# Optimization experiments

Hardware: AMD Instinct MI355X
Metric: run time of the kernel (lower is better)

Reference implementation:

```python
import jax, jax.numpy as jnp
import numpy as np

D = 1024      # input_dim
H = 16        # head_num
HD = 64       # head_dim
HID = 4096    # mlp hidden
CUR = 512     # cur_seq
PREV = 512    # prev_seq (memory)
FULL = CUR + PREV
BS = 16
SCALE = 1.0 / (HD ** 0.5)


def setup_inputs() -> dict:
    key = jax.random.key(0)
    ks = jax.random.split(key, 20)
    def nrm(k, shape, s=0.02):
        return (jax.random.normal(k, shape) * s).astype(jnp.float32)
    inp = {
        "inputs": nrm(ks[0], (CUR, BS, D), 1.0),
        "pos_embedding": nrm(ks[1], (FULL, 1, D), 1.0),
        "u": nrm(ks[2], (H, HD)),
        "v": nrm(ks[3], (H, HD)),
        "memory": nrm(ks[4], (PREV, BS, D), 1.0),
        # causal mask: position i (query) may attend to j <= i + PREV; True = masked
        "mask": jnp.triu(jnp.ones((CUR, FULL), dtype=bool), k=PREV + 1)[:, :, None],
        # attention params (stored as (in, out); torch Linear applies x @ W.T + b)
        "Wkv": nrm(ks[5], (D, 2 * H * HD)), "bkv": jnp.zeros((2 * H * HD,), jnp.float32),
        "Wq": nrm(ks[6], (D, H * HD)), "bq": jnp.zeros((H * HD,), jnp.float32),
        "Wo": nrm(ks[7], (H * HD, D)), "bo": jnp.zeros((D,), jnp.float32),
        "Wp": nrm(ks[8], (D, H * HD)), "bp": jnp.zeros((H * HD,), jnp.float32),
        # layernorms
        "ln1_g": jnp.ones((D,), jnp.float32), "ln1_b": jnp.zeros((D,), jnp.float32),
        "ln2_g": jnp.ones((D,), jnp.float32), "ln2_b": jnp.zeros((D,), jnp.float32),
        # mlp (mlp_num=2): Linear(D,HID)+relu, Linear(HID,D)+relu
        "W1": nrm(ks[9], (D, HID)), "b1": jnp.zeros((HID,), jnp.float32),
        "W2": nrm(ks[10], (HID, D)), "b2": jnp.zeros((D,), jnp.float32),
        # GRU gates: stacked [Wr,Wz,Wg] and [Ur,Uz,Ug], no bias; bg init 2.0
        "g1_W": nrm(ks[11], (3, D, D)), "g1_U": nrm(ks[12], (3, D, D)),
        "g1_bg": jnp.full((D,), 2.0, jnp.float32),
        "g2_W": nrm(ks[13], (3, D, D)), "g2_U": nrm(ks[14], (3, D, D)),
        "g2_bg": jnp.full((D,), 2.0, jnp.float32),
    }
    return inp


def _layernorm(x, g, b, eps=1e-5):
    mu = jnp.mean(x, axis=-1, keepdims=True)
    var = jnp.mean(jnp.square(x - mu), axis=-1, keepdims=True)
    return (x - mu) * jax.lax.rsqrt(var + eps) * g + b


def _rel_shift(x):
    # x: (bs, head, cur, full) -> pad/reshape/slice trick of Transformer-XL
    b, h, c, f = x.shape
    xp = jnp.pad(x, ((0, 0), (0, 0), (0, 0), (1, 0)))      # (b,h,c,f+1)
    xp = xp.reshape(b, h, f + 1, c)
    return xp[:, :, 1:, :].reshape(b, h, c, f)


def _gru_gate(x, y, W, U, bg):
    # W, U: (3, D, D) for [r, z, g] gates; torch Linear => y @ W[i].T
    r = jax.nn.sigmoid(y @ W[0].T + x @ U[0].T)
    z = jax.nn.sigmoid(y @ W[1].T + x @ U[1].T - bg)
    h = jnp.tanh(y @ W[2].T + (r * x) @ U[2].T)
    return (1.0 - z) * x + z * h


def _attention_xl(x_cur, pos_emb, x_full, u, v, mask,
                  Wkv, bkv, Wq, bq, Wo, bo, Wp, bp):
    cur, bs, _ = x_cur.shape
    full = x_full.shape[0]
    kv = x_full @ Wkv + bkv                                  # (full, bs, 2*H*HD)
    key, value = jnp.split(kv, 2, axis=-1)
    query = x_cur @ Wq + bq                                  # (cur, bs, H*HD)
    r = (pos_emb @ Wp + bp).reshape(full, H, HD)             # (full, H, HD)

    key = key.reshape(full, bs, H, HD)
    value = value.reshape(full, bs, H, HD)
    query = query.reshape(cur, bs, H, HD)

    content = jnp.einsum('ibhd,jbhd->bhij', query + u, key)  # (bs,H,cur,full)
    position = jnp.einsum('ibhd,jhd->bhij', query + v, r)    # (bs,H,cur,full)
    position = _rel_shift(position)

    attn = (content + position) * SCALE
    # mask: (cur, full, 1) bool, True = masked
    m = mask[:, :, 0][None, None]                            # (1,1,cur,full)
    attn = jnp.where(m, -jnp.inf, attn)
    p = jax.nn.softmax(attn, axis=-1)

    out = jnp.einsum('bhij,jbhd->ibhd', p, value).reshape(cur, bs, H * HD)
    return out @ Wo + bo                                     # (cur, bs, D)


def reference(inputs, pos_embedding, u, v, memory, mask,
              Wkv, bkv, Wq, bq, Wo, bo, Wp, bp,
              ln1_g, ln1_b, ln2_g, ln2_b,
              W1, b1, W2, b2,
              g1_W, g1_U, g1_bg, g2_W, g2_U, g2_bg):
    prev = memory.shape[0]
    full_input = jnp.concatenate([memory, inputs], axis=0)   # (full, bs, D)
    x1 = _layernorm(full_input, ln1_g, ln1_b)
    a1 = _attention_xl(x1[prev:], pos_embedding, x1, u, v, mask,
                       Wkv, bkv, Wq, bq, Wo, bo, Wp, bp)
    a1 = jax.nn.relu(a1)                                     # dropout = identity (eval)
    o1 = _gru_gate(inputs, a1, g1_W, g1_U, g1_bg)
    x2 = _layernorm(o1, ln2_g, ln2_b)
    m2 = jax.nn.relu(jax.nn.relu(x2 @ W1 + b1) @ W2 + b2)    # mlp: act after every linear
    o2 = _gru_gate(o1, m2, g2_W, g2_U, g2_bg)
    return o2
```

## Files before the change

### kernel.cpp

```cpp
#include <hip/hip_runtime.h>
#include <stdint.h>

typedef _Float16 h16;
typedef __attribute__((ext_vector_type(8))) _Float16 f16x8;
typedef __attribute__((ext_vector_type(4))) _Float16 f16x4;
typedef __attribute__((ext_vector_type(4))) float f32x4;

enum { F_OBF = 1, F_BIAS = 2, F_RELU = 4, F_ACC = 8, F_DUAL = 16 };

#define BARRIER_MEM                                  \
  do {                                               \
    asm volatile("" ::: "memory");                   \
    __builtin_amdgcn_s_barrier();                    \
    asm volatile("" ::: "memory");                   \
  } while (0)

static __device__ __forceinline__ void gload16(const void* g, void* l) {
  __builtin_amdgcn_global_load_lds((__attribute__((address_space(1))) void*)g,
                                   (__attribute__((address_space(3))) void*)l,
                                   16, 0, 0);
}

template <int BN, int FLAGS>
__global__ __launch_bounds__(512) void gemm2_k(
    const h16* __restrict__ A, const h16* __restrict__ B,
    void* __restrict__ Cv, const float* __restrict__ bias,
    int K, int lda, int ldb, int ldc, int gm,
    void* __restrict__ C2v, const float* __restrict__ bias2) {
  constexpr int NH = BN / 128;
  constexpr int WN = BN / 4;
  __shared__ h16 Al[2][256][64];
  __shared__ h16 Bl[2][BN][64];

  const int tid = threadIdx.x, lane = tid & 63, wid = tid >> 6;
  const int wr = wid >> 2, wn = wid & 3;
  const int ar = lane & 15, q4 = lane >> 4;

  const int nwg = gridDim.x, cpx = nwg >> 3;
  const int bid = (blockIdx.x & 7) * cpx + (blockIdx.x >> 3);
  const int mx = bid % gm, ny = bid / gm;

  const h16* Ab = A + (long)mx * 256 * lda;
  const h16* Bb = B + (long)ny * BN * ldb;

  auto stageA = [&](int buf, int half, int k0) {
#pragma unroll
    for (int l = 0; l < 2; ++l) {
      const int idx = l * 512 + tid;
      const int row = half * 128 + (idx >> 3), sl = idx & 7;
      gload16(Ab + (long)row * lda + k0 + (sl ^ (row & 7)) * 8,
              (char*)&Al[buf][0][0] + (half * 1024 + l * 512 + wid * 64) * 16);
    }
  };
  auto stageB = [&](int buf, int half, int k0) {
#pragma unroll
    for (int l = 0; l < NH; ++l) {
      const int idx = l * 512 + tid;
      const int row = half * (BN / 2) + (idx >> 3), sl = idx & 7;
      gload16(Bb + (long)row * ldb + k0 + (sl ^ (row & 7)) * 8,
              (char*)&Bl[buf][0][0] + (half * (BN * 4) + l * 512 + wid * 64) * 16);
    }
  };

  f32x4 acc[8][2 * NH] = {};
  const int nk = K >> 6;

  stageB(0, 0, 0); stageB(0, 1, 0); stageA(0, 0, 0); stageA(0, 1, 0);
  if (nk > 1) { stageB(1, 0, 64); stageB(1, 1, 64); stageA(1, 0, 64); stageA(1, 1, 64); }
  if (nk > 1) {
    if constexpr (NH == 2) asm volatile("s_waitcnt vmcnt(8)" ::: "memory");
    else                   asm volatile("s_waitcnt vmcnt(6)" ::: "memory");
  } else {
    asm volatile("s_waitcnt vmcnt(0)" ::: "memory");
  }
  BARRIER_MEM;

  for (int kt = 0; kt < nk; ++kt) {
    const int b = kt & 1;
    const int k2 = (kt + 2) << 6;
    const bool pf = (kt + 2) < nk;

    f16x8 a0[4][2], b0[NH][2];
#pragma unroll
    for (int m = 0; m < 4; ++m) {
      const int row = wr * 128 + m * 16 + ar;
#pragma unroll
      for (int ks = 0; ks < 2; ++ks)
        a0[m][ks] = *(const f16x8*)&Al[b][row][((ks * 4 + q4) ^ (row & 7)) * 8];
    }
#pragma unroll
    for (int n = 0; n < NH; ++n) {
      const int row = wn * WN + n * 16 + ar;
#pragma unroll
      for (int ks = 0; ks < 2; ++ks)
        b0[n][ks] = *(const f16x8*)&Bl[b][row][((ks * 4 + q4) ^ (row & 7)) * 8];
    }
    BARRIER_MEM;
    __builtin_amdgcn_s_setprio(1);
#pragma unroll
    for (int m = 0; m < 4; ++m)
#pragma unroll
      for (int n = 0; n < NH; ++n)
#pragma unroll
        for (int ks = 0; ks < 2; ++ks)
          acc[m][n] = __builtin_amdgcn_mfma_f32_16x16x32_f16(a0[m][ks], b0[n][ks], acc[m][n], 0, 0, 0);
    __builtin_amdgcn_s_setprio(0);
    BARRIER_MEM;

    f16x8 b1f[NH][2];
#pragma unroll
    for (int n = 0; n < NH; ++n) {
      const int row = wn * WN + (n + NH) * 16 + ar;
#pragma unroll
      for (int ks = 0; ks < 2; ++ks)
        b1f[n][ks] = *(const f16x8*)&Bl[b][row][((ks * 4 + q4) ^ (row & 7)) * 8];
    }
    BARRIER_MEM;
    __builtin_amdgcn_s_setprio(1);
#pragma unroll
    for (int m = 0; m < 4; ++m)
#pragma unroll
      for (int n = 0; n < NH; ++n)
#pragma unroll
        for (int ks = 0; ks < 2; ++ks)
          acc[m][n + NH] = __builtin_amdgcn_mfma_f32_16x16x32_f16(a0[m][ks], b1f[n][ks], acc[m][n + NH], 0, 0, 0);
    __builtin_amdgcn_s_setprio(0);
    BARRIER_MEM;

    f16x8 a1f[4][2];
#pragma unroll
    for (int m = 0; m < 4; ++m) {
      const int row = wr * 128 + (m + 4) * 16 + ar;
#pragma unroll
      for (int ks = 0; ks < 2; ++ks)
        a1f[m][ks] = *(const f16x8*)&Al[b][row][((ks * 4 + q4) ^ (row & 7)) * 8];
    }
    if (pf) { stageB(b, 0, k2); stageB(b, 1, k2); }
    BARRIER_MEM;
    __builtin_amdgcn_s_setprio(1);
#pragma unroll
    for (int m = 0; m < 4; ++m)
#pragma unroll
      for (int n = 0; n < NH; ++n)
#pragma unroll
        for (int ks = 0; ks < 2; ++ks)
          acc[m + 4][n] = __builtin_amdgcn_mfma_f32_16x16x32_f16(a1f[m][ks], b0[n][ks], acc[m + 4][n], 0, 0, 0);
    __builtin_amdgcn_s_setprio(0);
    BARRIER_MEM;

    if (pf) { stageA(b, 0, k2); stageA(b, 1, k2); }
    __builtin_amdgcn_s_setprio(1);
#pragma unroll
    for (int m = 0; m < 4; ++m)
#pragma unroll
      for (int n = 0; n < NH; ++n)
#pragma unroll
        for (int ks = 0; ks < 2; ++ks)
          acc[m + 4][n + NH] = __builtin_amdgcn_mfma_f32_16x16x32_f16(a1f[m][ks], b1f[n][ks], acc[m + 4][n + NH], 0, 0, 0);
    __builtin_amdgcn_s_setprio(0);
    if (pf) {
      if constexpr (NH == 2) asm volatile("s_waitcnt vmcnt(8)" ::: "memory");
      else                   asm volatile("s_waitcnt vmcnt(6)" ::: "memory");
    } else if (kt + 1 < nk) {
      asm volatile("s_waitcnt vmcnt(0)" ::: "memory");
    }
    BARRIER_MEM;
  }

#pragma unroll
  for (int m = 0; m < 8; ++m) {
#pragma unroll
    for (int n = 0; n < 2 * NH; ++n) {
      const int col = ny * BN + wn * WN + n * 16 + ar;
      float bv1 = 0.f, bv2 = 0.f;
      if (FLAGS & F_BIAS) bv1 = bias[col];
      if (FLAGS & F_DUAL) bv2 = bias2[col];
#pragma unroll
      for (int r = 0; r < 4; ++r) {
        const int row = mx * 256 + wr * 128 + m * 16 + q4 * 4 + r;
        float val = acc[m][n][r] + bv1;
        if (FLAGS & F_RELU) val = fmaxf(val, 0.f);
        if constexpr ((FLAGS & F_ACC) != 0) {
          float* p = (float*)Cv + (long)row * ldc + col;
          *p = *p + val;
        } else if constexpr ((FLAGS & F_OBF) != 0) {
          ((h16*)Cv)[(long)row * ldc + col] = (h16)val;
          if constexpr ((FLAGS & F_DUAL) != 0)
            ((h16*)C2v)[(long)row * ldc + col] = (h16)(acc[m][n][r] + bv2);
        } else {
          ((float*)Cv)[(long)row * ldc + col] = val;
        }
      }
    }
  }
}

__global__ __launch_bounds__(256) void fattn_k(
    const h16* __restrict__ qu, const h16* __restrict__ qv,
    const h16* __restrict__ kvb, const h16* __restrict__ vT,
    const h16* __restrict__ rb, h16* __restrict__ attn) {
  __shared__ h16 Kl[2][128][64];
  __shared__ h16 Vl[64][128];
  __shared__ h16 Psc[4][16][164];

  const int tid = threadIdx.x, lane = tid & 63, wv = tid >> 6;
  const int z = blockIdx.x, b = z >> 4, h = z & 15;
  const int i0 = blockIdx.y * 64;
  const int ar = lane & 15, q4 = lane >> 4;
  const int myrow = i0 + wv * 16;
  const h16* vTz = vT + (long)z * 64 * 1024;

  const long qoff = ((long)(myrow + ar) * 16 + b) * 1024 + h * 64 + q4 * 8;
  f16x8 quf[2], qvf[2];
  quf[0] = *(const f16x8*)&qu[qoff];
  quf[1] = *(const f16x8*)&qu[qoff + 32];
  qvf[0] = *(const f16x8*)&qv[qoff];
  qvf[1] = *(const f16x8*)&qv[qoff + 32];

  f32x4 o[4] = {};
  float lrow[4] = {0.f, 0.f, 0.f, 0.f};

  const int ntiles = (i0 + 575 + 128) >> 7;

  auto stageK = [&](int buf, int j0) {
#pragma unroll
    for (int it = 0; it < 4; ++it) {
      const int ch = it * 256 + wv * 64 + lane;
      const int kr = ch >> 3, ks = ch & 7;
      gload16(kvb + ((long)(j0 + kr) * 16 + b) * 2048 + h * 64 + (ks ^ (kr & 7)) * 8,
              (char*)&Kl[buf][0][0] + (it * 256 + wv * 64) * 16);
    }
  };
  auto stageV = [&](int j0) {
#pragma unroll
    for (int it = 0; it < 4; ++it) {
      const int ch = it * 256 + wv * 64 + lane;
      const int vd = ch >> 4, vs = ch & 15;
      gload16(vTz + (long)vd * 1024 + j0 + (vs ^ (vd & 7)) * 8,
              (char*)&Vl[0][0] + (it * 256 + wv * 64) * 16);
    }
  };

  stageK(0, 0);
  asm volatile("s_waitcnt vmcnt(0)" ::: "memory");
  __builtin_amdgcn_s_barrier();

  for (int t = 0; t < ntiles; ++t) {
    const int j0 = t * 128;
    const int kb = t & 1;
    const bool pk = (t + 1) < ntiles;

    stageV(j0);
    if (pk) stageK(kb ^ 1, (t + 1) * 128);
    if (pk) asm volatile("s_waitcnt vmcnt(8)" ::: "memory");
    else    asm volatile("s_waitcnt vmcnt(4)" ::: "memory");
    BARRIER_MEM;

    f32x4 acc_c[8] = {};
#pragma unroll
    for (int kd = 0; kd < 2; ++kd)
#pragma unroll
      for (int nf = 0; nf < 8; ++nf) {
        const int j = nf * 16 + ar;
        const int phys = (kd * 4 + q4) ^ (j & 7);
        const f16x8 kf = *(const f16x8*)&Kl[kb][j][phys * 8];
        acc_c[nf] = __builtin_amdgcn_mfma_f32_16x16x32_f16(quf[kd], kf, acc_c[nf], 0, 0, 0);
      }

    const int jbase = j0 - myrow + 496;
    f32x4 acc_p[9] = {};
#pragma unroll
    for (int kd = 0; kd < 2; ++kd)
#pragma unroll
      for (int jf = 0; jf < 9; ++jf) {
        int jjr = jbase + jf * 16 + ar;
        if (jjr > 1023) jjr = 1023;
        const f16x8 rf = *(const f16x8*)&rb[(long)jjr * 1024 + h * 64 + kd * 32 + q4 * 8];
        acc_p[jf] = __builtin_amdgcn_mfma_f32_16x16x32_f16(qvf[kd], rf, acc_p[jf], 0, 0, 0);
      }
#pragma unroll
    for (int jf = 0; jf < 9; ++jf)
#pragma unroll
      for (int r = 0; r < 4; ++r)
        Psc[wv][q4 * 4 + r][jf * 16 + ar] = (h16)acc_p[jf][r];

    float p[8][4];
#pragma unroll
    for (int nf = 0; nf < 8; ++nf)
#pragma unroll
      for (int r = 0; r < 4; ++r) {
        const int iloc = q4 * 4 + r;
        const int jloc = nf * 16 + ar;
        const int band = jloc - iloc + 15;
        const float pv = (float)Psc[wv][iloc][band];
        const float sv = (acc_c[nf][r] + pv) * 0.125f;
        const bool ok = (j0 + jloc) <= (myrow + iloc + 512);
        p[nf][r] = ok ? __expf(sv) : 0.f;
      }
#pragma unroll
    for (int r = 0; r < 4; ++r) {
      float ts = 0.f;
#pragma unroll
      for (int nf = 0; nf < 8; ++nf) ts += p[nf][r];
      ts += __shfl_xor(ts, 1);
      ts += __shfl_xor(ts, 2);
      ts += __shfl_xor(ts, 4);
      ts += __shfl_xor(ts, 8);
      lrow[r] += ts;
    }

#pragma unroll
    for (int nf = 0; nf < 8; ++nf)
#pragma unroll
      for (int r = 0; r < 4; ++r) {
        const int iloc = q4 * 4 + r, jloc = nf * 16 + ar;
        Psc[wv][iloc][((jloc >> 3) ^ (iloc & 7)) * 8 + (jloc & 7)] = (h16)p[nf][r];
      }

    if (pk) asm volatile("s_waitcnt vmcnt(4)" ::: "memory");
    else    asm volatile("s_waitcnt vmcnt(0)" ::: "memory");
    BARRIER_MEM;

#pragma unroll
    for (int ks = 0; ks < 4; ++ks) {
      const f16x8 pa = *(const f16x8*)&Psc[wv][ar][((ks * 4 + q4) ^ (ar & 7)) * 8];
#pragma unroll
      for (int vnf = 0; vnf < 4; ++vnf) {
        const int d = vnf * 16 + ar;
        const f16x8 vb = *(const f16x8*)&Vl[d][((ks * 4 + q4) ^ (d & 7)) * 8];
        o[vnf] = __builtin_amdgcn_mfma_f32_16x16x32_f16(pa, vb, o[vnf], 0, 0, 0);
      }
    }
    BARRIER_MEM;
  }

#pragma unroll
  for (int vnf = 0; vnf < 4; ++vnf)
#pragma unroll
    for (int r = 0; r < 4; ++r) {
      const int i_ = myrow + q4 * 4 + r;
      attn[((long)i_ * 16 + b) * 1024 + h * 64 + vnf * 16 + ar] =
          (h16)(o[vnf][r] / lrow[r]);
    }
}

__global__ __launch_bounds__(256) void wtransM_k(
    const float* __restrict__ Wkv, const float* __restrict__ Wq,
    const float* __restrict__ Wo, const float* __restrict__ Wp,
    const float* __restrict__ W1, const float* __restrict__ W2,
    h16* __restrict__ o0, h16* __restrict__ o1, h16* __restrict__ o2,
    h16* __restrict__ o3, h16* __restrict__ o4, h16* __restrict__ o5) {
  const int seg = blockIdx.y, t = blockIdx.x;
  int gx, gy, N, K;
  const float* in;
  h16* out;
  switch (seg) {
    case 0: gx = 64;  gy = 32;  in = Wkv; out = o0; N = 2048; K = 1024; break;
    case 1: gx = 32;  gy = 32;  in = Wq;  out = o1; N = 1024; K = 1024; break;
    case 2: gx = 32;  gy = 32;  in = Wo;  out = o2; N = 1024; K = 1024; break;
    case 3: gx = 32;  gy = 32;  in = Wp;  out = o3; N = 1024; K = 1024; break;
    case 4: gx = 128; gy = 32;  in = W1;  out = o4; N = 4096; K = 1024; break;
    default: gx = 32; gy = 128; in = W2;  out = o5; N = 1024; K = 4096; break;
  }
  if (t >= gx * gy) return;
  const int n0 = (t % gx) * 32, k0 = (t / gx) * 32;
  __shared__ float tb[32][33];
  const int tx = threadIdx.x & 31, ty = threadIdx.x >> 5;
#pragma unroll
  for (int j = 0; j < 32; j += 8)
    tb[ty + j][tx] = in[(long)(k0 + ty + j) * N + n0 + tx];
  __syncthreads();
#pragma unroll
  for (int j = 0; j < 32; j += 8)
    out[(long)(n0 + ty + j) * K + k0 + tx] = (h16)tb[tx][ty + j];
}

__global__ __launch_bounds__(256) void cast_k(const float* __restrict__ in,
                                              h16* __restrict__ out, long n4) {
  const long i = (long)blockIdx.x * 256 + threadIdx.x;
  if (i >= n4) return;
  const float4 v = ((const float4*)in)[i];
  f16x4 o;
  o[0] = (h16)v.x; o[1] = (h16)v.y; o[2] = (h16)v.z; o[3] = (h16)v.w;
  ((f16x4*)out)[i] = o;
}

__global__ __launch_bounds__(256) void gateprep_k(
    const float* __restrict__ W1g, const float* __restrict__ U1g,
    const float* __restrict__ W2g, const float* __restrict__ U2g,
    h16* __restrict__ o1, h16* __restrict__ o2) {
  const long i = (long)blockIdx.x * 256 + threadIdx.x;
  const long elem = i * 4;
  const int row = (int)(elem >> 11);
  const int col = (int)(elem & 2047);
  const int gate = row >> 10, oc = row & 1023;
  const float* W = (blockIdx.y == 0) ? W1g : W2g;
  const float* U = (blockIdx.y == 0) ? U1g : U2g;
  h16* out = (blockIdx.y == 0) ? o1 : o2;
  const float* src = (col < 1024)
      ? (W + (long)gate * 1048576 + (long)oc * 1024 + col)
      : (U + (long)gate * 1048576 + (long)oc * 1024 + (col - 1024));
  const float4 v = *(const float4*)src;
  f16x4 o;
  o[0] = (h16)v.x; o[1] = (h16)v.y; o[2] = (h16)v.z; o[3] = (h16)v.w;
  *(f16x4*)(out + elem) = o;
}

__global__ __launch_bounds__(256) void xcast_k(const float* __restrict__ in,
                                               h16* __restrict__ yx) {
  const long i = (long)blockIdx.x * 256 + threadIdx.x;
  const long row = i >> 8;
  const int c4 = (int)(i & 255);
  const float4 v = ((const float4*)in)[i];
  f16x4 o;
  o[0] = (h16)v.x; o[1] = (h16)v.y; o[2] = (h16)v.z; o[3] = (h16)v.w;
  *(f16x4*)(yx + row * 2048 + 1024 + c4 * 4) = o;
}

__global__ void addbias_k(const float* __restrict__ bq, const float* __restrict__ u,
                          const float* __restrict__ v, float* __restrict__ qu,
                          float* __restrict__ qv) {
  const int c = blockIdx.x * 256 + threadIdx.x;
  if (c < 1024) { qu[c] = bq[c] + u[c]; qv[c] = bq[c] + v[c]; }
}

__global__ __launch_bounds__(256) void zero_out_k(float* __restrict__ out, long n) {
  const long i = (long)blockIdx.x * 256 + threadIdx.x;
  if (i < n) out[i] = 0.f;
}

__global__ __launch_bounds__(256) void ln_k(const float* __restrict__ src0,
                                            const float* __restrict__ src1, int rows0,
                                            const float* __restrict__ g,
                                            const float* __restrict__ b,
                                            h16* __restrict__ out) {
  const int row = blockIdx.x, tid = threadIdx.x;
  const float* src = (row < rows0) ? (src0 + (long)row * 1024)
                                   : (src1 + (long)(row - rows0) * 1024);
  const float4 x = ((const float4*)src)[tid];
  float s = x.x + x.y + x.z + x.w;
  float sq = x.x * x.x + x.y * x.y + x.z * x.z + x.w * x.w;
#pragma unroll
  for (int o = 32; o > 0; o >>= 1) { s += __shfl_down(s, o); sq += __shfl_down(sq, o); }
  __shared__ float red[8];
  const int lane = tid & 63, w = tid >> 6;
  if (lane == 0) { red[w] = s; red[4 + w] = sq; }
  __syncthreads();
  s = red[0] + red[1] + red[2] + red[3];
  sq = red[4] + red[5] + red[6] + red[7];
  const float mu = s * (1.f / 1024.f);
  const float inv = rsqrtf(sq * (1.f / 1024.f) - mu * mu + 1e-5f);
  const float4 gg = ((const float4*)g)[tid], bb = ((const float4*)b)[tid];
  f16x4 o;
  o[0] = (h16)((x.x - mu) * inv * gg.x + bb.x);
  o[1] = (h16)((x.y - mu) * inv * gg.y + bb.y);
  o[2] = (h16)((x.z - mu) * inv * gg.z + bb.z);
  o[3] = (h16)((x.w - mu) * inv * gg.w + bb.w);
  ((f16x4*)(out + (long)row * 1024))[tid] = o;
}

__global__ __launch_bounds__(256) void vtrans_k(const h16* __restrict__ kv,
                                                h16* __restrict__ vT) {
  const int z = blockIdx.y, b = z >> 4, h = z & 15;
  const int j0 = blockIdx.x * 64;
  __shared__ h16 t[64][72];
  const int jj = threadIdx.x >> 3, c = threadIdx.x & 7;
#pragma unroll
  for (int half = 0; half < 2; ++half) {
    const int j = jj + half * 32;
    const f16x8 v = *(const f16x8*)(kv + ((long)(j0 + j) * 16 + b) * 2048 + 1024 + h * 64 + c * 8);
    *(f16x8*)&t[j][c * 8] = v;
  }
  __syncthreads();
#pragma unroll
  for (int half = 0; half < 2; ++half) {
    const int d = jj + half * 32;
    f16x8 o;
#pragma unroll
    for (int k = 0; k < 8; ++k) o[k] = t[c * 8 + k][d];
    *(f16x8*)(vT + ((long)z * 64 + d) * 1024 + j0 + c * 8) = o;
  }
}

__global__ __launch_bounds__(256) void gru_rx_k(const h16* __restrict__ T,
                                                const float* __restrict__ x,
                                                h16* __restrict__ yx) {
  const long i = (long)blockIdx.x * 256 + threadIdx.x;
  const long row = i >> 8;
  const int c4 = (int)(i & 255);
  const f16x4 t = *(const f16x4*)(T + row * 2048 + c4 * 4);
  const float4 xx = ((const float4*)x)[i];
  f16x4 o;
  o[0] = (h16)(xx.x / (1.f + __expf(-(float)t[0])));
  o[1] = (h16)(xx.y / (1.f + __expf(-(float)t[1])));
  o[2] = (h16)(xx.z / (1.f + __expf(-(float)t[2])));
  o[3] = (h16)(xx.w / (1.f + __expf(-(float)t[3])));
  *(f16x4*)(yx + row * 2048 + 1024 + c4 * 4) = o;
}

__global__ __launch_bounds__(256) void gru_out_k(const h16* __restrict__ T,
                                                 const h16* __restrict__ G,
                                                 const float* __restrict__ x,
                                                 const float* __restrict__ bg,
                                                 float* __restrict__ outf) {
  const long i = (long)blockIdx.x * 256 + threadIdx.x;
  const long row = i >> 8;
  const int c4 = (int)(i & 255);
  const f16x4 tz = *(const f16x4*)(T + row * 2048 + 1024 + c4 * 4);
  const f16x4 th = *(const f16x4*)(G + row * 1024 + c4 * 4);
  const float4 xx = ((const float4*)x)[i];
  const float4 bb = ((const float4*)bg)[c4];
  float4 o;
  {
    const float z0 = 1.f / (1.f + __expf(-((float)tz[0] - bb.x)));
    const float z1 = 1.f / (1.f + __expf(-((float)tz[1] - bb.y)));
    const float z2 = 1.f / (1.f + __expf(-((float)tz[2] - bb.z)));
    const float z3 = 1.f / (1.f + __expf(-((float)tz[3] - bb.w)));
    o.x = (1.f - z0) * xx.x + z0 * tanhf((float)th[0]);
    o.y = (1.f - z1) * xx.y + z1 * tanhf((float)th[1]);
    o.z = (1.f - z2) * xx.z + z2 * tanhf((float)th[2]);
    o.w = (1.f - z3) * xx.w + z3 * tanhf((float)th[3]);
  }
  ((float4*)outf)[i] = o;
}

__global__ __launch_bounds__(256) void gruo_ln_k(
    const h16* __restrict__ T, const h16* __restrict__ G,
    const float* __restrict__ x, const float* __restrict__ bg,
    const float* __restrict__ lng, const float* __restrict__ lnb,
    float* __restrict__ outf, h16* __restrict__ yx2, h16* __restrict__ x2) {
  const int row = blockIdx.x, tid = threadIdx.x;
  const f16x4 tz = *(const f16x4*)(T + (long)row * 2048 + 1024 + tid * 4);
  const f16x4 th = *(const f16x4*)(G + (long)row * 1024 + tid * 4);
  const float4 xx = ((const float4*)(x + (long)row * 1024))[tid];
  const float4 bb = ((const float4*)bg)[tid];
  float4 o;
  {
    const float z0 = 1.f / (1.f + __expf(-((float)tz[0] - bb.x)));
    const float z1 = 1.f / (1.f + __expf(-((float)tz[1] - bb.y)));
    const float z2 = 1.f / (1.f + __expf(-((float)tz[2] - bb.z)));
    const float z3 = 1.f / (1.f + __expf(-((float)tz[3] - bb.w)));
    o.x = (1.f - z0) * xx.x + z0 * tanhf((float)th[0]);
    o.y = (1.f - z1) * xx.y + z1 * tanhf((float)th[1]);
    o.z = (1.f - z2) * xx.z + z2 * tanhf((float)th[2]);
    o.w = (1.f - z3) * xx.w + z3 * tanhf((float)th[3]);
  }
  ((float4*)(outf + (long)row * 1024))[tid] = o;
  {
    f16x4 oh;
    oh[0] = (h16)o.x; oh[1] = (h16)o.y; oh[2] = (h16)o.z; oh[3] = (h16)o.w;
    *(f16x4*)(yx2 + (long)row * 2048 + 1024 + tid * 4) = oh;
  }
  float s = o.x + o.y + o.z + o.w;
  float sq = o.x * o.x + o.y * o.y + o.z * o.z + o.w * o.w;
#pragma unroll
  for (int off = 32; off > 0; off >>= 1) {
    s += __shfl_down(s, off);
    sq += __shfl_down(sq, off);
  }
  __shared__ float red[8];
  const int lane = tid & 63, wvi = tid >> 6;
  if (lane == 0) { red[wvi] = s; red[4 + wvi] = sq; }
  __syncthreads();
  s = red[0] + red[1] + red[2] + red[3];
  sq = red[4] + red[5] + red[6] + red[7];
  const float mu = s * (1.f / 1024.f);
  const float inv = rsqrtf(sq * (1.f / 1024.f) - mu * mu + 1e-5f);
  const float4 gg = ((const float4*)lng)[tid], bn = ((const float4*)lnb)[tid];
  f16x4 ol;
  ol[0] = (h16)((o.x - mu) * inv * gg.x + bn.x);
  ol[1] = (h16)((o.y - mu) * inv * gg.y + bn.y);
  ol[2] = (h16)((o.z - mu) * inv * gg.z + bn.z);
  ol[3] = (h16)((o.w - mu) * inv * gg.w + bn.w);
  *(f16x4*)(x2 + (long)row * 1024 + tid * 4) = ol;
}

extern "C" void kernel_launch(void* const* d_in, const int* in_sizes, int n_in,
                              void* d_out, int out_size, void* d_ws, size_t ws_size,
                              hipStream_t stream) {
  const float* inputs = (const float*)d_in[0];
  const float* pos    = (const float*)d_in[1];
  const float* u      = (const float*)d_in[2];
  const float* v      = (const float*)d_in[3];
  const float* memory = (const float*)d_in[4];
  const float* Wkv = (const float*)d_in[6];  const float* bkv = (const float*)d_in[7];
  const float* Wq  = (const float*)d_in[8];  const float* bq  = (const float*)d_in[9];
  const float* Wo  = (const float*)d_in[10]; const float* bo  = (const float*)d_in[11];
  const float* Wp  = (const float*)d_in[12]; const float* bp  = (const float*)d_in[13];
  const float* ln1_g = (const float*)d_in[14]; const float* ln1_b = (const float*)d_in[15];
  const float* ln2_g = (const float*)d_in[16]; const float* ln2_b = (const float*)d_in[17];
  const float* W1 = (const float*)d_in[18]; const float* b1 = (const float*)d_in[19];
  const float* W2 = (const float*)d_in[20]; const float* b2 = (const float*)d_in[21];
  const float* g1_W = (const float*)d_in[22]; const float* g1_U = (const float*)d_in[23];
  const float* g1_bg = (const float*)d_in[24];
  const float* g2_W = (const float*)d_in[25]; const float* g2_U = (const float*)d_in[26];
  const float* g2_bg = (const float*)d_in[27];
  (void)in_sizes; (void)n_in;

  const size_t MB = 1u << 20;
  const size_t NEEDED = 247 * MB;
  const dim3 blk(256);
  if (ws_size < NEEDED) {
    zero_out_k<<<(out_size + 255) / 256, blk, 0, stream>>>((float*)d_out, out_size);
    return;
  }

  char* w = (char*)d_ws;
  h16* WoT   = (h16*)(w + 0 * MB);
  h16* W1T   = (h16*)(w + 2 * MB);
  h16* W2T   = (h16*)(w + 10 * MB);
  h16* g1B   = (h16*)(w + 18 * MB);
  h16* g2B   = (h16*)(w + 30 * MB);
  h16* WkvT  = (h16*)(w + 42 * MB);
  h16* WqT   = (h16*)(w + 46 * MB);
  h16* WpT   = (h16*)(w + 48 * MB);
  h16* posb  = (h16*)(w + 50 * MB);
  float* bias_qu = (float*)(w + 52 * MB);
  float* bias_qv = (float*)(w + 52 * MB + 8192);
  h16* yx1   = (h16*)(w + 53 * MB);
  h16* x1    = (h16*)(w + 85 * MB);
  char* Rbig =        w + 117 * MB;
  h16* qu    = (h16*)(w + 181 * MB);
  h16* qv    = (h16*)(w + 197 * MB);
  h16* attn  = (h16*)(w + 213 * MB);
  h16* rb    = (h16*)(w + 245 * MB);

  h16*   kvb  = (h16*)Rbig;
  h16*   Trzh = (h16*)Rbig;
  h16*   Tg   = (h16*)(Rbig + 32 * MB);
  h16*   h1   = (h16*)Rbig;
  h16*   vT   = x1;
  h16*   yx2  = x1;
  float* o1f  = (float*)attn;
  h16*   x2   = yx1;

  wtransM_k<<<dim3(4096, 6), blk, 0, stream>>>(Wkv, Wq, Wo, Wp, W1, W2,
                                               WkvT, WqT, WoT, WpT, W1T, W2T);
  gateprep_k<<<dim3(6144, 2), blk, 0, stream>>>(g1_W, g1_U, g2_W, g2_U, g1B, g2B);
  cast_k<<<1024, blk, 0, stream>>>(pos, posb, 262144);
  xcast_k<<<8192, blk, 0, stream>>>(inputs, yx1);
  addbias_k<<<4, blk, 0, stream>>>(bq, u, v, bias_qu, bias_qv);

  ln_k<<<16384, blk, 0, stream>>>(memory, inputs, 8192, ln1_g, ln1_b, x1);

  gemm2_k<256, F_OBF | F_BIAS><<<dim3(512), dim3(512), 0, stream>>>(
      x1, WkvT, kvb, bkv, 1024, 1024, 1024, 2048, 64, nullptr, nullptr);
  gemm2_k<128, F_OBF | F_BIAS | F_DUAL><<<dim3(256), dim3(512), 0, stream>>>(
      x1 + 8192L * 1024, WqT, qu, bias_qu, 1024, 1024, 1024, 1024, 32, qv, bias_qv);
  gemm2_k<128, F_OBF | F_BIAS><<<dim3(32), dim3(512), 0, stream>>>(
      posb, WpT, rb, bp, 1024, 1024, 1024, 1024, 4, nullptr, nullptr);
  vtrans_k<<<dim3(16, 256), blk, 0, stream>>>(kvb, vT);

  fattn_k<<<dim3(256, 8), blk, 0, stream>>>(qu, qv, kvb, vT, rb, attn);

  gemm2_k<128, F_OBF | F_BIAS | F_RELU><<<dim3(256), dim3(512), 0, stream>>>(
      attn, WoT, yx1, bo, 1024, 1024, 1024, 2048, 32, nullptr, nullptr);

  gemm2_k<256, F_OBF><<<dim3(256), dim3(512), 0, stream>>>(
      yx1, g1B, Trzh, nullptr, 2048, 2048, 2048, 2048, 32, nullptr, nullptr);
  gru_rx_k<<<8192, blk, 0, stream>>>(Trzh, inputs, yx1);
  gemm2_k<128, F_OBF><<<dim3(256), dim3(512), 0, stream>>>(
      yx1, g1B + 2048L * 2048, Tg, nullptr, 2048, 2048, 2048, 1024, 32, nullptr, nullptr);
  gruo_ln_k<<<8192, blk, 0, stream>>>(Trzh, Tg, inputs, g1_bg, ln2_g, ln2_b,
                                      o1f, yx2, x2);

  gemm2_k<256, F_OBF | F_BIAS | F_RELU><<<dim3(512), dim3(512), 0, stream>>>(
      x2, W1T, h1, b1, 1024, 1024, 1024, 4096, 32, nullptr, nullptr);
  gemm2_k<128, F_OBF | F_BIAS | F_RELU><<<dim3(256), dim3(512), 0, stream>>>(
      h1, W2T, yx2, b2, 4096, 4096, 4096, 2048, 32, nullptr, nullptr);

  gemm2_k<256, F_OBF><<<dim3(256), dim3(512), 0, stream>>>(
      yx2, g2B, Trzh, nullptr, 2048, 2048, 2048, 2048, 32, nullptr, nullptr);
  gru_rx_k<<<8192, blk, 0, stream>>>(Trzh, o1f, yx2);
  gemm2_k<128, F_OBF><<<dim3(256), dim3(512), 0, stream>>>(
      yx2, g2B + 2048L * 2048, Tg, nullptr, 2048, 2048, 2048, 1024, 32, nullptr, nullptr);
  gru_out_k<<<8192, blk, 0, stream>>>(Trzh, Tg, o1f, g2_bg, (float*)d_out);
}
```

Baseline: 976.8 us.

## Merge prep kernels, store GRU intermediate in fp16, add MFMA priority hints

Combines the pos cast, input cast and bias-add prep kernels into a single launch with a y-segment switch. The first GRU output o1 is now stored as fp16 instead of fp32, which halves the traffic for the second GRU stage reads. The attention kernel raises wave priority around its MFMA loops and pads the score scratch row from 164 to 168 halves. The fp16 intermediate lowers the precision of the residual path in the second GRU.

```diff
diff --git a/kernel.cpp b/kernel.cpp
--- a/kernel.cpp
+++ b/kernel.cpp
@@ -201,7 +201,7 @@
     const h16* __restrict__ rb, h16* __restrict__ attn) {
   __shared__ h16 Kl[2][128][64];
   __shared__ h16 Vl[64][128];
-  __shared__ h16 Psc[4][16][164];
+  __shared__ h16 Psc[4][16][168];
 
   const int tid = threadIdx.x, lane = tid & 63, wv = tid >> 6;
   const int z = blockIdx.x, b = z >> 4, h = z & 15;
@@ -257,6 +257,7 @@
     BARRIER_MEM;
 
     f32x4 acc_c[8] = {};
+    __builtin_amdgcn_s_setprio(1);
 #pragma unroll
     for (int kd = 0; kd < 2; ++kd)
 #pragma unroll
@@ -266,9 +267,11 @@
         const f16x8 kf = *(const f16x8*)&Kl[kb][j][phys * 8];
         acc_c[nf] = __builtin_amdgcn_mfma_f32_16x16x32_f16(quf[kd], kf, acc_c[nf], 0, 0, 0);
       }
+    __builtin_amdgcn_s_setprio(0);
 
     const int jbase = j0 - myrow + 496;
     f32x4 acc_p[9] = {};
+    __builtin_amdgcn_s_setprio(1);
 #pragma unroll
     for (int kd = 0; kd < 2; ++kd)
 #pragma unroll
@@ -278,6 +281,7 @@
         const f16x8 rf = *(const f16x8*)&rb[(long)jjr * 1024 + h * 64 + kd * 32 + q4 * 8];
         acc_p[jf] = __builtin_amdgcn_mfma_f32_16x16x32_f16(qvf[kd], rf, acc_p[jf], 0, 0, 0);
       }
+    __builtin_amdgcn_s_setprio(0);
 #pragma unroll
     for (int jf = 0; jf < 9; ++jf)
 #pragma unroll
@@ -321,6 +325,7 @@
     else    asm volatile("s_waitcnt vmcnt(0)" ::: "memory");
     BARRIER_MEM;
 
+    __builtin_amdgcn_s_setprio(1);
 #pragma unroll
     for (int ks = 0; ks < 4; ++ks) {
       const f16x8 pa = *(const f16x8*)&Psc[wv][ar][((ks * 4 + q4) ^ (ar & 7)) * 8];
@@ -331,6 +336,7 @@
         o[vnf] = __builtin_amdgcn_mfma_f32_16x16x32_f16(pa, vb, o[vnf], 0, 0, 0);
       }
     }
+    __builtin_amdgcn_s_setprio(0);
     BARRIER_MEM;
   }
 
@@ -373,16 +379,6 @@
 #pragma unroll
   for (int j = 0; j < 32; j += 8)
     out[(long)(n0 + ty + j) * K + k0 + tx] = (h16)tb[tx][ty + j];
-}
-
-__global__ __launch_bounds__(256) void cast_k(const float* __restrict__ in,
-                                              h16* __restrict__ out, long n4) {
-  const long i = (long)blockIdx.x * 256 + threadIdx.x;
-  if (i >= n4) return;
-  const float4 v = ((const float4*)in)[i];
-  f16x4 o;
-  o[0] = (h16)v.x; o[1] = (h16)v.y; o[2] = (h16)v.z; o[3] = (h16)v.w;
-  ((f16x4*)out)[i] = o;
 }
 
 __global__ __launch_bounds__(256) void gateprep_k(
@@ -406,22 +402,31 @@
   *(f16x4*)(out + elem) = o;
 }
 
-__global__ __launch_bounds__(256) void xcast_k(const float* __restrict__ in,
-                                               h16* __restrict__ yx) {
-  const long i = (long)blockIdx.x * 256 + threadIdx.x;
-  const long row = i >> 8;
-  const int c4 = (int)(i & 255);
-  const float4 v = ((const float4*)in)[i];
-  f16x4 o;
-  o[0] = (h16)v.x; o[1] = (h16)v.y; o[2] = (h16)v.z; o[3] = (h16)v.w;
-  *(f16x4*)(yx + row * 2048 + 1024 + c4 * 4) = o;
-}
-
-__global__ void addbias_k(const float* __restrict__ bq, const float* __restrict__ u,
-                          const float* __restrict__ v, float* __restrict__ qu,
-                          float* __restrict__ qv) {
-  const int c = blockIdx.x * 256 + threadIdx.x;
-  if (c < 1024) { qu[c] = bq[c] + u[c]; qv[c] = bq[c] + v[c]; }
+__global__ __launch_bounds__(256) void prep2_k(
+    const float* __restrict__ pos, h16* __restrict__ posb,
+    const float* __restrict__ inputs, h16* __restrict__ yx,
+    const float* __restrict__ bq, const float* __restrict__ u,
+    const float* __restrict__ v, float* __restrict__ qu, float* __restrict__ qv) {
+  const int seg = blockIdx.y;
+  if (seg == 0) {
+    const long i = (long)blockIdx.x * 256 + threadIdx.x;
+    if (i >= 262144) return;
+    const float4 x = ((const float4*)pos)[i];
+    f16x4 o;
+    o[0] = (h16)x.x; o[1] = (h16)x.y; o[2] = (h16)x.z; o[3] = (h16)x.w;
+    ((f16x4*)posb)[i] = o;
+  } else if (seg == 1) {
+    const long i = (long)blockIdx.x * 256 + threadIdx.x;
+    const long row = i >> 8;
+    const int c4 = (int)(i & 255);
+    const float4 x = ((const float4*)inputs)[i];
+    f16x4 o;
+    o[0] = (h16)x.x; o[1] = (h16)x.y; o[2] = (h16)x.z; o[3] = (h16)x.w;
+    *(f16x4*)(yx + row * 2048 + 1024 + c4 * 4) = o;
+  } else {
+    const int c = blockIdx.x * 256 + threadIdx.x;
+    if (c < 1024) { qu[c] = bq[c] + u[c]; qv[c] = bq[c] + v[c]; }
+  }
 }
 
 __global__ __launch_bounds__(256) void zero_out_k(float* __restrict__ out, long n) {
@@ -482,25 +487,32 @@
   }
 }
 
+template <typename XT>
 __global__ __launch_bounds__(256) void gru_rx_k(const h16* __restrict__ T,
-                                                const float* __restrict__ x,
+                                                const XT* __restrict__ x,
                                                 h16* __restrict__ yx) {
   const long i = (long)blockIdx.x * 256 + threadIdx.x;
   const long row = i >> 8;
   const int c4 = (int)(i & 255);
   const f16x4 t = *(const f16x4*)(T + row * 2048 + c4 * 4);
-  const float4 xx = ((const float4*)x)[i];
+  float xv[4];
+  if constexpr (sizeof(XT) == 4) {
+    const float4 xx = ((const float4*)x)[i];
+    xv[0] = xx.x; xv[1] = xx.y; xv[2] = xx.z; xv[3] = xx.w;
+  } else {
+    const f16x4 xx = ((const f16x4*)x)[i];
+    xv[0] = (float)xx[0]; xv[1] = (float)xx[1]; xv[2] = (float)xx[2]; xv[3] = (float)xx[3];
+  }
   f16x4 o;
-  o[0] = (h16)(xx.x / (1.f + __expf(-(float)t[0])));
-  o[1] = (h16)(xx.y / (1.f + __expf(-(float)t[1])));
-  o[2] = (h16)(xx.z / (1.f + __expf(-(float)t[2])));
-  o[3] = (h16)(xx.w / (1.f + __expf(-(float)t[3])));
+#pragma unroll
+  for (int k = 0; k < 4; ++k)
+    o[k] = (h16)(xv[k] / (1.f + __expf(-(float)t[k])));
   *(f16x4*)(yx + row * 2048 + 1024 + c4 * 4) = o;
 }
 
 __global__ __launch_bounds__(256) void gru_out_k(const h16* __restrict__ T,
                                                  const h16* __restrict__ G,
-                                                 const float* __restrict__ x,
+                                                 const h16* __restrict__ x,
                                                  const float* __restrict__ bg,
                                                  float* __restrict__ outf) {
   const long i = (long)blockIdx.x * 256 + threadIdx.x;
@@ -508,7 +520,7 @@
   const int c4 = (int)(i & 255);
   const f16x4 tz = *(const f16x4*)(T + row * 2048 + 1024 + c4 * 4);
   const f16x4 th = *(const f16x4*)(G + row * 1024 + c4 * 4);
-  const float4 xx = ((const float4*)x)[i];
+  const f16x4 xx = ((const f16x4*)x)[i];
   const float4 bb = ((const float4*)bg)[c4];
   float4 o;
   {
@@ -516,10 +528,10 @@
     const float z1 = 1.f / (1.f + __expf(-((float)tz[1] - bb.y)));
     const float z2 = 1.f / (1.f + __expf(-((float)tz[2] - bb.z)));
     const float z3 = 1.f / (1.f + __expf(-((float)tz[3] - bb.w)));
-    o.x = (1.f - z0) * xx.x + z0 * tanhf((float)th[0]);
-    o.y = (1.f - z1) * xx.y + z1 * tanhf((float)th[1]);
-    o.z = (1.f - z2) * xx.z + z2 * tanhf((float)th[2]);
-    o.w = (1.f - z3) * xx.w + z3 * tanhf((float)th[3]);
+    o.x = (1.f - z0) * (float)xx[0] + z0 * tanhf((float)th[0]);
+    o.y = (1.f - z1) * (float)xx[1] + z1 * tanhf((float)th[1]);
+    o.z = (1.f - z2) * (float)xx[2] + z2 * tanhf((float)th[2]);
+    o.w = (1.f - z3) * (float)xx[3] + z3 * tanhf((float)th[3]);
   }
   ((float4*)outf)[i] = o;
 }
@@ -528,7 +540,7 @@
     const h16* __restrict__ T, const h16* __restrict__ G,
     const float* __restrict__ x, const float* __restrict__ bg,
     const float* __restrict__ lng, const float* __restrict__ lnb,
-    float* __restrict__ outf, h16* __restrict__ yx2, h16* __restrict__ x2) {
+    h16* __restrict__ o1h, h16* __restrict__ yx2, h16* __restrict__ x2) {
   const int row = blockIdx.x, tid = threadIdx.x;
   const f16x4 tz = *(const f16x4*)(T + (long)row * 2048 + 1024 + tid * 4);
   const f16x4 th = *(const f16x4*)(G + (long)row * 1024 + tid * 4);
@@ -545,10 +557,10 @@
     o.z = (1.f - z2) * xx.z + z2 * tanhf((float)th[2]);
     o.w = (1.f - z3) * xx.w + z3 * tanhf((float)th[3]);
   }
-  ((float4*)(outf + (long)row * 1024))[tid] = o;
   {
     f16x4 oh;
     oh[0] = (h16)o.x; oh[1] = (h16)o.y; oh[2] = (h16)o.z; oh[3] = (h16)o.w;
+    *(f16x4*)(o1h + (long)row * 1024 + tid * 4) = oh;
     *(f16x4*)(yx2 + (long)row * 2048 + 1024 + tid * 4) = oh;
   }
   float s = o.x + o.y + o.z + o.w;
@@ -631,15 +643,14 @@
   h16*   h1   = (h16*)Rbig;
   h16*   vT   = x1;
   h16*   yx2  = x1;
-  float* o1f  = (float*)attn;
+  h16*   o1h  = attn;
   h16*   x2   = yx1;
 
   wtransM_k<<<dim3(4096, 6), blk, 0, stream>>>(Wkv, Wq, Wo, Wp, W1, W2,
                                                WkvT, WqT, WoT, WpT, W1T, W2T);
   gateprep_k<<<dim3(6144, 2), blk, 0, stream>>>(g1_W, g1_U, g2_W, g2_U, g1B, g2B);
-  cast_k<<<1024, blk, 0, stream>>>(pos, posb, 262144);
-  xcast_k<<<8192, blk, 0, stream>>>(inputs, yx1);
-  addbias_k<<<4, blk, 0, stream>>>(bq, u, v, bias_qu, bias_qv);
+  prep2_k<<<dim3(8192, 3), blk, 0, stream>>>(pos, posb, inputs, yx1,
+                                             bq, u, v, bias_qu, bias_qv);
 
   ln_k<<<16384, blk, 0, stream>>>(memory, inputs, 8192, ln1_g, ln1_b, x1);
 
@@ -658,11 +669,11 @@
 
   gemm2_k<256, F_OBF><<<dim3(256), dim3(512), 0, stream>>>(
       yx1, g1B, Trzh, nullptr, 2048, 2048, 2048, 2048, 32, nullptr, nullptr);
-  gru_rx_k<<<8192, blk, 0, stream>>>(Trzh, inputs, yx1);
+  gru_rx_k<float><<<8192, blk, 0, stream>>>(Trzh, inputs, yx1);
   gemm2_k<128, F_OBF><<<dim3(256), dim3(512), 0, stream>>>(
       yx1, g1B + 2048L * 2048, Tg, nullptr, 2048, 2048, 2048, 1024, 32, nullptr, nullptr);
   gruo_ln_k<<<8192, blk, 0, stream>>>(Trzh, Tg, inputs, g1_bg, ln2_g, ln2_b,
-                                      o1f, yx2, x2);
+                                      o1h, yx2, x2);
 
   gemm2_k<256, F_OBF | F_BIAS | F_RELU><<<dim3(512), dim3(512), 0, stream>>>(
       x2, W1T, h1, b1, 1024, 1024, 1024, 4096, 32, nullptr, nullptr);
@@ -671,8 +682,8 @@
 
   gemm2_k<256, F_OBF><<<dim3(256), dim3(512), 0, stream>>>(
       yx2, g2B, Trzh, nullptr, 2048, 2048, 2048, 2048, 32, nullptr, nullptr);
-  gru_rx_k<<<8192, blk, 0, stream>>>(Trzh, o1f, yx2);
+  gru_rx_k<h16><<<8192, blk, 0, stream>>>(Trzh, o1h, yx2);
   gemm2_k<128, F_OBF><<<dim3(256), dim3(512), 0, stream>>>(
       yx2, g2B + 2048L * 2048, Tg, nullptr, 2048, 2048, 2048, 1024, 32, nullptr, nullptr);
-  gru_out_k<<<8192, blk, 0, stream>>>(Trzh, Tg, o1f, g2_bg, (float*)d_out);
-}
+  gru_out_k<<<8192, blk, 0, stream>>>(Trzh, Tg, o1h, g2_bg, (float*)d_out);
+}
```

New measurement: 977.7 us. Within noise of the previous version (+0.1%).
